# Optimization experiments

Hardware: AMD Instinct MI355X
Metric: run time of the kernel (lower is better)

## Reference

```python
import jax, jax.numpy as jnp
import numpy as np

BN_INV = 1.0 / np.sqrt(1.0 + 1e-5)  # eval-mode BatchNorm1d with running_mean=0, running_var=1


def _lin_bn_relu(x, W, g, b):
    # Linear(no bias) -> BN(eval) -> ReLU
    return jax.nn.relu((x @ W.T) * (g * BN_INV) + b)


def setup_inputs() -> dict:
    key = jax.random.key(0)
    ks = jax.random.split(key, 24)
    B, P, N, C, H, OUT = 8, 1024, 20, 32, 256, 256
    s = 0.05
    inp = {
        "polylines": jax.random.normal(ks[0], (B, P, N, C), dtype=jnp.float32),
        "polylines_mask": jax.random.randint(ks[1], (B, P, N), 0, 2) > 0,
        # pre_mlps: [Lin(C->H,no bias)+BN+ReLU] x2, Lin(H->H, bias)
        "pre_w0": jax.random.normal(ks[2], (H, C), dtype=jnp.float32) * s,
        "pre_g0": jnp.ones((H,), jnp.float32),
        "pre_b0": jnp.zeros((H,), jnp.float32),
        "pre_w1": jax.random.normal(ks[3], (H, H), dtype=jnp.float32) * s,
        "pre_g1": jnp.ones((H,), jnp.float32),
        "pre_b1": jnp.zeros((H,), jnp.float32),
        "pre_w2": jax.random.normal(ks[4], (H, H), dtype=jnp.float32) * s,
        "pre_bias2": jnp.zeros((H,), jnp.float32),
        # mlps: c_in=2H -> [H,H,H]
        "mlp_w0": jax.random.normal(ks[5], (H, 2 * H), dtype=jnp.float32) * s,
        "mlp_g0": jnp.ones((H,), jnp.float32),
        "mlp_b0": jnp.zeros((H,), jnp.float32),
        "mlp_w1": jax.random.normal(ks[6], (H, H), dtype=jnp.float32) * s,
        "mlp_g1": jnp.ones((H,), jnp.float32),
        "mlp_b1": jnp.zeros((H,), jnp.float32),
        "mlp_w2": jax.random.normal(ks[7], (H, H), dtype=jnp.float32) * s,
        "mlp_bias2": jnp.zeros((H,), jnp.float32),
        # out_mlps (without_norm): Lin(H->H,bias)+ReLU, Lin(H->OUT,bias)
        "out_w0": jax.random.normal(ks[8], (H, H), dtype=jnp.float32) * s,
        "out_b0": jnp.zeros((H,), jnp.float32),
        "out_w1": jax.random.normal(ks[9], (OUT, H), dtype=jnp.float32) * s,
        "out_b1": jnp.zeros((OUT,), jnp.float32),
    }
    return inp


def reference(polylines, polylines_mask,
              pre_w0, pre_g0, pre_b0, pre_w1, pre_g1, pre_b1, pre_w2, pre_bias2,
              mlp_w0, mlp_g0, mlp_b0, mlp_w1, mlp_g1, mlp_b1, mlp_w2, mlp_bias2,
              out_w0, out_b0, out_w1, out_b1):
    # gather->MLP->zero-scatter is equivalent to dense MLP followed by mask-zeroing
    # (all per-point ops are elementwise / last-dim matmuls).
    m = polylines_mask[..., None].astype(polylines.dtype)  # (B,P,N,1)

    x = _lin_bn_relu(polylines, pre_w0, pre_g0, pre_b0)
    x = _lin_bn_relu(x, pre_w1, pre_g1, pre_b1)
    x = (x @ pre_w2.T + pre_bias2) * m                      # (B,P,N,H) zero at invalid

    pooled = x.max(axis=2)                                  # (B,P,H) max over zero-filled buffer
    x = jnp.concatenate(
        [x, jnp.broadcast_to(pooled[:, :, None, :], x.shape)], axis=-1)  # (B,P,N,2H)

    x = _lin_bn_relu(x, mlp_w0, mlp_g0, mlp_b0)
    x = _lin_bn_relu(x, mlp_w1, mlp_g1, mlp_b1)
    x = (x @ mlp_w2.T + mlp_bias2) * m                      # (B,P,N,H)

    buf = x.max(axis=2)                                     # (B,P,H)

    valid = jnp.any(polylines_mask, axis=-1)                # sum(mask)>0
    y = jax.nn.relu(buf @ out_w0.T + out_b0)
    y = (y @ out_w1.T + out_b1) * valid[..., None].astype(buf.dtype)  # (B,P,OUT)
    return y
```

## Files before the change

### kernel.cpp

```cpp
#include <hip/hip_runtime.h>
#include <stdint.h>
#include <stddef.h>

typedef __bf16 bf16;
typedef __bf16 bf16x4 __attribute__((ext_vector_type(4)));
typedef __bf16 bf16x8 __attribute__((ext_vector_type(8)));
typedef float f32x4 __attribute__((ext_vector_type(4)));
typedef float f32x16 __attribute__((ext_vector_type(16)));

#define BNI 0.9999950000374996f
#define NROW 240
#define NPOLYB 12
#define TOTROW 163840
#define NPOLY 8192
#define NBLK 683

#define AADDR(r, ch) ((r)*256 + ((((ch) ^ ((r)&31)))<<3))

#define OFF_ACT  0
#define OFF_WB0  122880
#define OFF_T2   155648
#define OFF_VAL  161792
#define LDS_TOTAL 161840

#define WS_PRE_W0 0
#define WS_PRE_W1 8192
#define WS_PRE_W2 73728
#define WS_MLP_W0 139264
#define WS_MLP_W1 270336
#define WS_MLP_W2 335872
#define WS_OUT_W0 401408
#define WS_OUT_W1 466944

__device__ __forceinline__ bf16 f2b(float f){
  unsigned int i = __builtin_bit_cast(unsigned int, f);
  unsigned int r = i + 0x7fffu + ((i >> 16) & 1u);
  unsigned short h = (unsigned short)(r >> 16);
  return __builtin_bit_cast(bf16, h);
}
__device__ __forceinline__ float b2f(bf16 x){
  unsigned short u = __builtin_bit_cast(unsigned short, x);
  union { unsigned int i; float f; } v; v.i = ((unsigned int)u) << 16; return v.f;
}
__device__ __forceinline__ bf16x8 ld8f(const float* p, float sc){
  f32x4 a = *(const f32x4*)p;
  f32x4 b = *(const f32x4*)(p + 4);
  bf16x8 r;
  #pragma unroll
  for (int j = 0; j < 4; ++j){ r[j] = f2b(a[j]*sc); r[4+j] = f2b(b[j]*sc); }
  return r;
}

__global__ __launch_bounds__(256)
void prep_kernel(const float* s0, const float* s1, const float* s2, const float* s3,
                 const float* s4, const float* s5, const float* s6, const float* s7,
                 const float* g0, const float* g1, const float* g3, const float* g4,
                 bf16* dst)
{
  const int offs[8] = {WS_PRE_W0, WS_PRE_W1, WS_PRE_W2, WS_MLP_W0,
                       WS_MLP_W1, WS_MLP_W2, WS_OUT_W0, WS_OUT_W1};
  const int sz[8]   = {8192, 65536, 65536, 131072, 65536, 65536, 65536, 65536};
  const int ld[8]   = {32, 256, 256, 512, 256, 256, 256, 256};
  int r = blockIdx.y;
  const float* src = s0;
  if (r == 1) src = s1; else if (r == 2) src = s2; else if (r == 3) src = s3;
  else if (r == 4) src = s4; else if (r == 5) src = s5; else if (r == 6) src = s6;
  else if (r == 7) src = s7;
  const float* gp = (r==0)?g0:(r==1)?g1:(r==3)?g3:(r==4)?g4:nullptr;
  int i = (blockIdx.x*256 + threadIdx.x)*8;
  if (i < sz[r]){
    float sc = gp ? gp[i/ld[r]]*BNI : 1.0f;
    *(bf16x8*)&dst[offs[r] + i] = ld8f(src + i, sc);
  }
}

__device__ __forceinline__ void stageAsyncG2(const bf16* W, int ldK, int tile, int kh,
                                             bf16* buf, int rp, int lane){
  #pragma unroll
  for (int i = 0; i < 2; ++i){
    int id = rp*128 + i*64 + lane;
    int fr = id >> 4, kcd = id & 15;
    int kcs = kcd ^ (fr & 15);
    const bf16* gsrc = W + (size_t)(tile*32 + fr)*ldK + kh*128 + kcs*8;
    bf16* l = buf + (size_t)(rp*128 + i*64)*8;
    __builtin_amdgcn_global_load_lds(
        (const __attribute__((address_space(1))) void*)gsrc,
        (__attribute__((address_space(3))) void*)l,
        16, 0, 0);
  }
}

template<int RELU, int MASK, int ADDT2>
__device__ __forceinline__ void epiT(
    const f32x16& acc, int nt, int row, int poly, float mk, bool valid,
    bf16* sAct, const bf16* sT2, const float* bptr, int hi)
{
  #pragma unroll
  for (int q2 = 0; q2 < 4; ++q2){
    int f0 = nt*32 + 8*q2 + 4*hi;
    f32x4 bb = *(const f32x4*)(bptr + f0);
    bf16x4 tv = {};
    if (ADDT2) tv = *(const bf16x4*)&sT2[poly*256 + f0];
    bf16x4 o;
    #pragma unroll
    for (int j = 0; j < 4; ++j){
      float v = acc[4*q2 + j];
      if (ADDT2) v += b2f(tv[j]);
      v += bb[j];
      if (RELU) v = fmaxf(v, 0.0f);
      if (MASK) v *= mk;
      o[j] = f2b(v);
    }
    if (valid)
      *(bf16x4*)&sAct[row*256 + (((nt*4 + q2) ^ (row & 31))<<3) + 4*hi] = o;
  }
}

template<int RELU, int MASK, int ADDT2>
__device__ __forceinline__ void layerR2(
    bf16* sAct, bf16* wbase, const bf16* sT2,
    const bf16* W, int ldK, const float* bptr,
    const int* maskp, int blk, int g, int rp, int row0, int row1,
    int rowc0, int rowc1, int lane32, int hi, int lane)
{
  bf16x8 B0[16], B1[16];
  #pragma unroll
  for (int t = 0; t < 16; ++t){
    B0[t] = *(const bf16x8*)&sAct[AADDR(rowc0, 2*t + hi)];
    B1[t] = *(const bf16x8*)&sAct[AADDR(rowc1, 2*t + hi)];
  }
  float mk0 = 1.0f, mk1 = 1.0f;
  if (MASK){
    int g0 = blk*NROW + row0, g1 = blk*NROW + row1;
    mk0 = (row0 < NROW && g0 < TOTROW && maskp[g0]) ? 1.0f : 0.0f;
    mk1 = (row1 < NROW && g1 < TOTROW && maskp[g1]) ? 1.0f : 0.0f;
  }
  const int poly0 = rowc0/20, poly1 = rowc1/20;
  const bool valid0 = row0 < NROW, valid1 = row1 < NROW;
  bf16* bufA = wbase + (size_t)(2*g)*4096;
  bf16* bufB = bufA + 4096;

  stageAsyncG2(W, ldK, g*4, 0, bufA, rp, lane);
  __syncthreads();
  #pragma unroll 1
  for (int p = 0; p < 4; ++p){
    f32x16 acc0, acc1;
    stageAsyncG2(W, ldK, g*4 + p, 1, bufB, rp, lane);
    {
      const bf16* base = bufA + lane32*128;
      #pragma unroll
      for (int j = 0; j < 16; ++j){ acc0[j] = 0.0f; acc1[j] = 0.0f; }
      #pragma unroll
      for (int t = 0; t < 8; ++t){
        bf16x8 wf = *(const bf16x8*)(base + (((2*t + hi) ^ (lane32 & 15))<<3));
        acc0 = __builtin_amdgcn_mfma_f32_32x32x16_bf16(wf, B0[t], acc0, 0, 0, 0);
        acc1 = __builtin_amdgcn_mfma_f32_32x32x16_bf16(wf, B1[t], acc1, 0, 0, 0);
      }
    }
    __syncthreads();
    if (p < 3) stageAsyncG2(W, ldK, g*4 + p + 1, 0, bufA, rp, lane);
    {
      const bf16* base = bufB + lane32*128;
      #pragma unroll
      for (int t = 0; t < 8; ++t){
        bf16x8 wf = *(const bf16x8*)(base + (((2*t + hi) ^ (lane32 & 15))<<3));
        acc0 = __builtin_amdgcn_mfma_f32_32x32x16_bf16(wf, B0[8 + t], acc0, 0, 0, 0);
        acc1 = __builtin_amdgcn_mfma_f32_32x32x16_bf16(wf, B1[8 + t], acc1, 0, 0, 0);
      }
      epiT<RELU,MASK,ADDT2>(acc0, g*4 + p, row0, poly0, mk0, valid0, sAct, sT2, bptr, hi);
      epiT<RELU,MASK,ADDT2>(acc1, g*4 + p, row1, poly1, mk1, valid1, sAct, sT2, bptr, hi);
    }
    __syncthreads();
  }
}

__device__ __forceinline__ void poolT(const bf16* sAct, bf16* sPool, int tid){
  if (tid < 384){
    int poly = tid >> 5, c = tid & 31;
    float m[8];
    bf16x8 v0 = *(const bf16x8*)&sAct[AADDR(poly*20, c)];
    #pragma unroll
    for (int j = 0; j < 8; ++j) m[j] = b2f(v0[j]);
    for (int r = 1; r < 20; ++r){
      bf16x8 v = *(const bf16x8*)&sAct[AADDR(poly*20 + r, c)];
      #pragma unroll
      for (int j = 0; j < 8; ++j) m[j] = fmaxf(m[j], b2f(v[j]));
    }
    bf16x8 o;
    #pragma unroll
    for (int j = 0; j < 8; ++j) o[j] = f2b(m[j]);
    *(bf16x8*)&sPool[AADDR(poly, c)] = o;
  }
}

__global__ __launch_bounds__(512) __attribute__((amdgpu_waves_per_eu(1, 2)))
void traj_kernel(const float* __restrict__ poly, const int* __restrict__ maskp,
                 const float* pre_b0, const float* pre_b1, const float* pre_bias2,
                 const float* mlp_b0, const float* mlp_b1, const float* mlp_bias2,
                 const float* out_b0, const float* out_b1,
                 const bf16* __restrict__ ws,
                 float* __restrict__ outp)
{
  extern __shared__ char smem[];
  bf16*  sAct   = (bf16*)(smem + OFF_ACT);
  bf16*  wbase  = (bf16*)(smem + OFF_WB0);
  bf16*  sT2    = (bf16*)(smem + OFF_T2);
  float* sValid = (float*)(smem + OFF_VAL);
  bf16*  sPool  = wbase;
  bf16*  sY     = sAct;

  const int tid = threadIdx.x;
  const int w = tid >> 6, L = tid & 63, lane32 = L & 31, hi = L >> 5;
  const int g = w >> 2, rp = w & 3;
  const int row0 = rp*64 + lane32;
  const int row1 = row0 + 32;
  const int rowc0 = row0 < NROW ? row0 : NROW - 1;
  const int rowc1 = row1 < NROW ? row1 : NROW - 1;
  const int blk = blockIdx.x;

  const bf16* pw0 = ws + WS_PRE_W0;
  const bf16* pw1 = ws + WS_PRE_W1;
  const bf16* pw2 = ws + WS_PRE_W2;
  const bf16* mw0 = ws + WS_MLP_W0;
  const bf16* mw1 = ws + WS_MLP_W1;
  const bf16* mw2 = ws + WS_MLP_W2;
  const bf16* ow0 = ws + WS_OUT_W0;
  const bf16* ow1 = ws + WS_OUT_W1;

  #pragma unroll
  for (int i = 0; i < 2; ++i){
    int id = tid + 512*i;
    if (id < 960){
      int r = id >> 2, c = id & 3;
      int grow = blk*NROW + r;
      bf16x8 v = {};
      if (grow < TOTROW) v = ld8f(poly + (size_t)grow*32 + c*8, 1.0f);
      *(bf16x8*)&sAct[AADDR(r, c)] = v;
    }
  }
  __syncthreads();
  if (tid < NPOLYB){
    float v = 0.0f;
    #pragma unroll
    for (int r = 0; r < 20; ++r){
      int gg = blk*NROW + tid*20 + r;
      if (gg < TOTROW && maskp[gg]) v = 1.0f;
    }
    sValid[tid] = v;
  }

  {
    bf16x8 B00 = *(const bf16x8*)&sAct[AADDR(rowc0, hi)];
    bf16x8 B01 = *(const bf16x8*)&sAct[AADDR(rowc0, 2 + hi)];
    bf16x8 B10 = *(const bf16x8*)&sAct[AADDR(rowc1, hi)];
    bf16x8 B11 = *(const bf16x8*)&sAct[AADDR(rowc1, 2 + hi)];
    __syncthreads();
    #pragma unroll 1
    for (int ntl = 0; ntl < 4; ++ntl){
      int nt = g*4 + ntl;
      const bf16* p = pw0 + (size_t)(nt*32 + lane32)*32 + 8*hi;
      bf16x8 w0 = *(const bf16x8*)p;
      bf16x8 w1 = *(const bf16x8*)(p + 16);
      f32x16 acc0 = {}, acc1 = {};
      acc0 = __builtin_amdgcn_mfma_f32_32x32x16_bf16(w0, B00, acc0, 0, 0, 0);
      acc0 = __builtin_amdgcn_mfma_f32_32x32x16_bf16(w1, B01, acc0, 0, 0, 0);
      acc1 = __builtin_amdgcn_mfma_f32_32x32x16_bf16(w0, B10, acc1, 0, 0, 0);
      acc1 = __builtin_amdgcn_mfma_f32_32x32x16_bf16(w1, B11, acc1, 0, 0, 0);
      epiT<1,0,0>(acc0, nt, row0, 0, 1.0f, row0 < NROW, sAct, sT2, pre_b0, hi);
      epiT<1,0,0>(acc1, nt, row1, 0, 1.0f, row1 < NROW, sAct, sT2, pre_b0, hi);
    }
  }
  __syncthreads();

  layerR2<1,0,0>(sAct, wbase, sT2, pw1, 256, pre_b1,    maskp, blk, g, rp, row0, row1, rowc0, rowc1, lane32, hi, L);
  layerR2<0,1,0>(sAct, wbase, sT2, pw2, 256, pre_bias2, maskp, blk, g, rp, row0, row1, rowc0, rowc1, lane32, hi, L);

  poolT(sAct, sPool, tid);
  __syncthreads();

  {
    bf16x8 Bp[16];
    #pragma unroll
    for (int t = 0; t < 16; ++t)
      Bp[t] = *(const bf16x8*)&sPool[AADDR((lane32 < NPOLYB ? lane32 : 0), 2*t + hi)];
    int nt = w;
    const bf16* p = mw0 + (size_t)(nt*32 + lane32)*512 + 256 + 8*hi;
    f32x16 acc = {};
    #pragma unroll
    for (int t = 0; t < 16; ++t){
      bf16x8 wf = *(const bf16x8*)(p + 16*t);
      acc = __builtin_amdgcn_mfma_f32_32x32x16_bf16(wf, Bp[t], acc, 0, 0, 0);
    }
    if (lane32 < NPOLYB){
      #pragma unroll
      for (int q2 = 0; q2 < 4; ++q2){
        int f0 = nt*32 + 8*q2 + 4*hi;
        bf16x4 o;
        #pragma unroll
        for (int j = 0; j < 4; ++j) o[j] = f2b(acc[4*q2 + j]);
        *(bf16x4*)&sT2[lane32*256 + f0] = o;
      }
    }
  }
  __syncthreads();

  layerR2<1,0,1>(sAct, wbase, sT2, mw0, 512, mlp_b0,    maskp, blk, g, rp, row0, row1, rowc0, rowc1, lane32, hi, L);
  layerR2<1,0,0>(sAct, wbase, sT2, mw1, 256, mlp_b1,    maskp, blk, g, rp, row0, row1, rowc0, rowc1, lane32, hi, L);
  layerR2<0,1,0>(sAct, wbase, sT2, mw2, 256, mlp_bias2, maskp, blk, g, rp, row0, row1, rowc0, rowc1, lane32, hi, L);

  poolT(sAct, sPool, tid);
  __syncthreads();

  {
    bf16x8 Bp[16];
    #pragma unroll
    for (int t = 0; t < 16; ++t)
      Bp[t] = *(const bf16x8*)&sPool[AADDR((lane32 < NPOLYB ? lane32 : 0), 2*t + hi)];
    int nt = w;
    const bf16* p = ow0 + (size_t)(nt*32 + lane32)*256 + 8*hi;
    f32x16 acc = {};
    #pragma unroll
    for (int t = 0; t < 16; ++t){
      bf16x8 wf = *(const bf16x8*)(p + 16*t);
      acc = __builtin_amdgcn_mfma_f32_32x32x16_bf16(wf, Bp[t], acc, 0, 0, 0);
    }
    if (lane32 < NPOLYB){
      #pragma unroll
      for (int q2 = 0; q2 < 4; ++q2){
        int f0 = nt*32 + 8*q2 + 4*hi;
        f32x4 bb = *(const f32x4*)(out_b0 + f0);
        bf16x4 o;
        #pragma unroll
        for (int j = 0; j < 4; ++j) o[j] = f2b(fmaxf(acc[4*q2 + j] + bb[j], 0.0f));
        *(bf16x4*)&sY[lane32*256 + (((nt*4 + q2) ^ (lane32 & 31))<<3) + 4*hi] = o;
      }
    }
  }
  __syncthreads();

  {
    bf16x8 By[16];
    #pragma unroll
    for (int t = 0; t < 16; ++t)
      By[t] = *(const bf16x8*)&sY[AADDR((lane32 < NPOLYB ? lane32 : 0), 2*t + hi)];
    int gp = blk*NPOLYB + lane32;
    float vd = (lane32 < NPOLYB) ? sValid[lane32] : 0.0f;
    int nt = w;
    const bf16* p = ow1 + (size_t)(nt*32 + lane32)*256 + 8*hi;
    f32x16 acc = {};
    #pragma unroll
    for (int t = 0; t < 16; ++t){
      bf16x8 wf = *(const bf16x8*)(p + 16*t);
      acc = __builtin_amdgcn_mfma_f32_32x32x16_bf16(wf, By[t], acc, 0, 0, 0);
    }
    if (lane32 < NPOLYB && gp < NPOLY){
      #pragma unroll
      for (int q2 = 0; q2 < 4; ++q2){
        int f0 = nt*32 + 8*q2 + 4*hi;
        f32x4 bb = *(const f32x4*)(out_b1 + f0);
        f32x4 o;
        #pragma unroll
        for (int j = 0; j < 4; ++j) o[j] = (acc[4*q2 + j] + bb[j]) * vd;
        *(f32x4*)&outp[(size_t)gp*256 + f0] = o;
      }
    }
  }
}

extern "C" void kernel_launch(void* const* d_in, const int* in_sizes, int n_in,
                              void* d_out, int out_size, void* d_ws, size_t ws_size,
                              hipStream_t stream)
{
  const float* poly      = (const float*)d_in[0];
  const int*   maskp     = (const int*)  d_in[1];
  const float* pre_w0    = (const float*)d_in[2];
  const float* pre_g0    = (const float*)d_in[3];
  const float* pre_b0    = (const float*)d_in[4];
  const float* pre_w1    = (const float*)d_in[5];
  const float* pre_g1    = (const float*)d_in[6];
  const float* pre_b1    = (const float*)d_in[7];
  const float* pre_w2    = (const float*)d_in[8];
  const float* pre_bias2 = (const float*)d_in[9];
  const float* mlp_w0    = (const float*)d_in[10];
  const float* mlp_g0    = (const float*)d_in[11];
  const float* mlp_b0    = (const float*)d_in[12];
  const float* mlp_w1    = (const float*)d_in[13];
  const float* mlp_g1    = (const float*)d_in[14];
  const float* mlp_b1    = (const float*)d_in[15];
  const float* mlp_w2    = (const float*)d_in[16];
  const float* mlp_bias2 = (const float*)d_in[17];
  const float* out_w0    = (const float*)d_in[18];
  const float* out_b0    = (const float*)d_in[19];
  const float* out_w1    = (const float*)d_in[20];
  const float* out_b1    = (const float*)d_in[21];

  bf16* ws = (bf16*)d_ws;

  (void)hipFuncSetAttribute((const void*)&traj_kernel,
                            hipFuncAttributeMaxDynamicSharedMemorySize, LDS_TOTAL);

  prep_kernel<<<dim3(64, 8), dim3(256), 0, stream>>>(
      pre_w0, pre_w1, pre_w2, mlp_w0, mlp_w1, mlp_w2, out_w0, out_w1,
      pre_g0, pre_g1, mlp_g0, mlp_g1, ws);

  traj_kernel<<<dim3(NBLK), dim3(512), LDS_TOTAL, stream>>>(
      poly, maskp,
      pre_b0, pre_b1, pre_bias2,
      mlp_b0, mlp_b1, mlp_bias2,
      out_b0, out_b1,
      ws, (float*)d_out);
}
```

Before: 325.8 us.

## Halve block tile to 120 rows with 256 threads and quarter-K weight staging

Each block now processes 6 polylines (120 rows) with 4 waves instead of 12 polylines with 8 waves. LDS use drops to about 80KB, so two blocks can fit per CU, and the grid doubles to 1366 blocks. Weight tiles are now staged in four 64-wide K chunks with smaller double buffers. Each wave also loops over two output column tiles in the pooled and output stages. The intent is higher occupancy and better latency hiding, at the cost of more barriers per layer and weights being reloaded across twice as many blocks.

```diff
diff --git a/kernel.cpp b/kernel.cpp
--- a/kernel.cpp
+++ b/kernel.cpp
@@ -9,19 +9,19 @@
 typedef float f32x16 __attribute__((ext_vector_type(16)));
 
 #define BNI 0.9999950000374996f
-#define NROW 240
-#define NPOLYB 12
+#define NROW 120
+#define NPOLYB 6
 #define TOTROW 163840
 #define NPOLY 8192
-#define NBLK 683
+#define NBLK 1366
 
 #define AADDR(r, ch) ((r)*256 + ((((ch) ^ ((r)&31)))<<3))
 
 #define OFF_ACT  0
-#define OFF_WB0  122880
-#define OFF_T2   155648
-#define OFF_VAL  161792
-#define LDS_TOTAL 161840
+#define OFF_WB   61440
+#define OFF_T2   77824
+#define OFF_VAL  80896
+#define LDS_TOTAL 80920
 
 #define WS_PRE_W0 0
 #define WS_PRE_W1 8192
@@ -74,19 +74,32 @@
   }
 }
 
-__device__ __forceinline__ void stageAsyncG2(const bf16* W, int ldK, int tile, int kh,
-                                             bf16* buf, int rp, int lane){
+__device__ __forceinline__ void stageAsyncQ(const bf16* W, int ldK, int tile, int kq,
+                                            bf16* buf, int rp, int lane){
   #pragma unroll
   for (int i = 0; i < 2; ++i){
     int id = rp*128 + i*64 + lane;
-    int fr = id >> 4, kcd = id & 15;
-    int kcs = kcd ^ (fr & 15);
-    const bf16* gsrc = W + (size_t)(tile*32 + fr)*ldK + kh*128 + kcs*8;
+    int fr = id >> 3, kcd = id & 7;
+    int kcs = kcd ^ (fr & 7);
+    const bf16* gsrc = W + (size_t)(tile*32 + fr)*ldK + kq*64 + kcs*8;
     bf16* l = buf + (size_t)(rp*128 + i*64)*8;
     __builtin_amdgcn_global_load_lds(
         (const __attribute__((address_space(1))) void*)gsrc,
         (__attribute__((address_space(3))) void*)l,
         16, 0, 0);
+  }
+}
+
+template<int KQ>
+__device__ __forceinline__ void mfma4(const bf16* buf, int lane32, int hi,
+                                      const bf16x8 (&B0)[16], const bf16x8 (&B1)[16],
+                                      f32x16& acc0, f32x16& acc1){
+  const bf16* base = buf + lane32*64;
+  #pragma unroll
+  for (int s = 0; s < 4; ++s){
+    bf16x8 wf = *(const bf16x8*)(base + (((2*s + hi) ^ (lane32 & 7))<<3));
+    acc0 = __builtin_amdgcn_mfma_f32_32x32x16_bf16(wf, B0[4*KQ + s], acc0, 0, 0, 0);
+    acc1 = __builtin_amdgcn_mfma_f32_32x32x16_bf16(wf, B1[4*KQ + s], acc1, 0, 0, 0);
   }
 }
 
@@ -117,7 +130,7 @@
 }
 
 template<int RELU, int MASK, int ADDT2>
-__device__ __forceinline__ void layerR2(
+__device__ __forceinline__ void layerQ(
     bf16* sAct, bf16* wbase, const bf16* sT2,
     const bf16* W, int ldK, const float* bptr,
     const int* maskp, int blk, int g, int rp, int row0, int row1,
@@ -137,45 +150,35 @@
   }
   const int poly0 = rowc0/20, poly1 = rowc1/20;
   const bool valid0 = row0 < NROW, valid1 = row1 < NROW;
-  bf16* bufA = wbase + (size_t)(2*g)*4096;
-  bf16* bufB = bufA + 4096;
-
-  stageAsyncG2(W, ldK, g*4, 0, bufA, rp, lane);
+  bf16* bufA = wbase + (size_t)(2*g)*2048;
+  bf16* bufB = bufA + 2048;
+
+  stageAsyncQ(W, ldK, g*4, 0, bufA, rp, lane);
   __syncthreads();
   #pragma unroll 1
   for (int p = 0; p < 4; ++p){
     f32x16 acc0, acc1;
-    stageAsyncG2(W, ldK, g*4 + p, 1, bufB, rp, lane);
-    {
-      const bf16* base = bufA + lane32*128;
-      #pragma unroll
-      for (int j = 0; j < 16; ++j){ acc0[j] = 0.0f; acc1[j] = 0.0f; }
-      #pragma unroll
-      for (int t = 0; t < 8; ++t){
-        bf16x8 wf = *(const bf16x8*)(base + (((2*t + hi) ^ (lane32 & 15))<<3));
-        acc0 = __builtin_amdgcn_mfma_f32_32x32x16_bf16(wf, B0[t], acc0, 0, 0, 0);
-        acc1 = __builtin_amdgcn_mfma_f32_32x32x16_bf16(wf, B1[t], acc1, 0, 0, 0);
-      }
-    }
+    #pragma unroll
+    for (int j = 0; j < 16; ++j){ acc0[j] = 0.0f; acc1[j] = 0.0f; }
+    stageAsyncQ(W, ldK, g*4 + p, 1, bufB, rp, lane);
+    mfma4<0>(bufA, lane32, hi, B0, B1, acc0, acc1);
     __syncthreads();
-    if (p < 3) stageAsyncG2(W, ldK, g*4 + p + 1, 0, bufA, rp, lane);
-    {
-      const bf16* base = bufB + lane32*128;
-      #pragma unroll
-      for (int t = 0; t < 8; ++t){
-        bf16x8 wf = *(const bf16x8*)(base + (((2*t + hi) ^ (lane32 & 15))<<3));
-        acc0 = __builtin_amdgcn_mfma_f32_32x32x16_bf16(wf, B0[8 + t], acc0, 0, 0, 0);
-        acc1 = __builtin_amdgcn_mfma_f32_32x32x16_bf16(wf, B1[8 + t], acc1, 0, 0, 0);
-      }
-      epiT<RELU,MASK,ADDT2>(acc0, g*4 + p, row0, poly0, mk0, valid0, sAct, sT2, bptr, hi);
-      epiT<RELU,MASK,ADDT2>(acc1, g*4 + p, row1, poly1, mk1, valid1, sAct, sT2, bptr, hi);
-    }
+    stageAsyncQ(W, ldK, g*4 + p, 2, bufA, rp, lane);
+    mfma4<1>(bufB, lane32, hi, B0, B1, acc0, acc1);
     __syncthreads();
+    stageAsyncQ(W, ldK, g*4 + p, 3, bufB, rp, lane);
+    mfma4<2>(bufA, lane32, hi, B0, B1, acc0, acc1);
+    __syncthreads();
+    if (p < 3) stageAsyncQ(W, ldK, g*4 + p + 1, 0, bufA, rp, lane);
+    mfma4<3>(bufB, lane32, hi, B0, B1, acc0, acc1);
+    epiT<RELU,MASK,ADDT2>(acc0, g*4 + p, row0, poly0, mk0, valid0, sAct, sT2, bptr, hi);
+    epiT<RELU,MASK,ADDT2>(acc1, g*4 + p, row1, poly1, mk1, valid1, sAct, sT2, bptr, hi);
+    __syncthreads();
   }
 }
 
 __device__ __forceinline__ void poolT(const bf16* sAct, bf16* sPool, int tid){
-  if (tid < 384){
+  if (tid < 192){
     int poly = tid >> 5, c = tid & 31;
     float m[8];
     bf16x8 v0 = *(const bf16x8*)&sAct[AADDR(poly*20, c)];
@@ -193,7 +196,7 @@
   }
 }
 
-__global__ __launch_bounds__(512) __attribute__((amdgpu_waves_per_eu(1, 2)))
+__global__ __launch_bounds__(256) __attribute__((amdgpu_waves_per_eu(1, 2)))
 void traj_kernel(const float* __restrict__ poly, const int* __restrict__ maskp,
                  const float* pre_b0, const float* pre_b1, const float* pre_bias2,
                  const float* mlp_b0, const float* mlp_b1, const float* mlp_bias2,
@@ -203,7 +206,7 @@
 {
   extern __shared__ char smem[];
   bf16*  sAct   = (bf16*)(smem + OFF_ACT);
-  bf16*  wbase  = (bf16*)(smem + OFF_WB0);
+  bf16*  wbase  = (bf16*)(smem + OFF_WB);
   bf16*  sT2    = (bf16*)(smem + OFF_T2);
   float* sValid = (float*)(smem + OFF_VAL);
   bf16*  sPool  = wbase;
@@ -211,7 +214,7 @@
 
   const int tid = threadIdx.x;
   const int w = tid >> 6, L = tid & 63, lane32 = L & 31, hi = L >> 5;
-  const int g = w >> 2, rp = w & 3;
+  const int g = w >> 1, rp = w & 1;
   const int row0 = rp*64 + lane32;
   const int row1 = row0 + 32;
   const int rowc0 = row0 < NROW ? row0 : NROW - 1;
@@ -229,8 +232,8 @@
 
   #pragma unroll
   for (int i = 0; i < 2; ++i){
-    int id = tid + 512*i;
-    if (id < 960){
+    int id = tid + 256*i;
+    if (id < 480){
       int r = id >> 2, c = id & 3;
       int grow = blk*NROW + r;
       bf16x8 v = {};
@@ -272,8 +275,8 @@
   }
   __syncthreads();
 
-  layerR2<1,0,0>(sAct, wbase, sT2, pw1, 256, pre_b1,    maskp, blk, g, rp, row0, row1, rowc0, rowc1, lane32, hi, L);
-  layerR2<0,1,0>(sAct, wbase, sT2, pw2, 256, pre_bias2, maskp, blk, g, rp, row0, row1, rowc0, rowc1, lane32, hi, L);
+  layerQ<1,0,0>(sAct, wbase, sT2, pw1, 256, pre_b1,    maskp, blk, g, rp, row0, row1, rowc0, rowc1, lane32, hi, L);
+  layerQ<0,1,0>(sAct, wbase, sT2, pw2, 256, pre_bias2, maskp, blk, g, rp, row0, row1, rowc0, rowc1, lane32, hi, L);
 
   poolT(sAct, sPool, tid);
   __syncthreads();
@@ -283,30 +286,33 @@
     #pragma unroll
     for (int t = 0; t < 16; ++t)
       Bp[t] = *(const bf16x8*)&sPool[AADDR((lane32 < NPOLYB ? lane32 : 0), 2*t + hi)];
-    int nt = w;
-    const bf16* p = mw0 + (size_t)(nt*32 + lane32)*512 + 256 + 8*hi;
-    f32x16 acc = {};
-    #pragma unroll
-    for (int t = 0; t < 16; ++t){
-      bf16x8 wf = *(const bf16x8*)(p + 16*t);
-      acc = __builtin_amdgcn_mfma_f32_32x32x16_bf16(wf, Bp[t], acc, 0, 0, 0);
-    }
-    if (lane32 < NPOLYB){
+    #pragma unroll 1
+    for (int it = 0; it < 2; ++it){
+      int nt = w + 4*it;
+      const bf16* p = mw0 + (size_t)(nt*32 + lane32)*512 + 256 + 8*hi;
+      f32x16 acc = {};
       #pragma unroll
-      for (int q2 = 0; q2 < 4; ++q2){
-        int f0 = nt*32 + 8*q2 + 4*hi;
-        bf16x4 o;
+      for (int t = 0; t < 16; ++t){
+        bf16x8 wf = *(const bf16x8*)(p + 16*t);
+        acc = __builtin_amdgcn_mfma_f32_32x32x16_bf16(wf, Bp[t], acc, 0, 0, 0);
+      }
+      if (lane32 < NPOLYB){
         #pragma unroll
-        for (int j = 0; j < 4; ++j) o[j] = f2b(acc[4*q2 + j]);
-        *(bf16x4*)&sT2[lane32*256 + f0] = o;
-      }
-    }
-  }
-  __syncthreads();
-
-  layerR2<1,0,1>(sAct, wbase, sT2, mw0, 512, mlp_b0,    maskp, blk, g, rp, row0, row1, rowc0, rowc1, lane32, hi, L);
-  layerR2<1,0,0>(sAct, wbase, sT2, mw1, 256, mlp_b1,    maskp, blk, g, rp, row0, row1, rowc0, rowc1, lane32, hi, L);
-  layerR2<0,1,0>(sAct, wbase, sT2, mw2, 256, mlp_bias2, maskp, blk, g, rp, row0, row1, rowc0, rowc1, lane32, hi, L);
+        for (int q2 = 0; q2 < 4; ++q2){
+          int f0 = nt*32 + 8*q2 + 4*hi;
+          bf16x4 o;
+          #pragma unroll
+          for (int j = 0; j < 4; ++j) o[j] = f2b(acc[4*q2 + j]);
+          *(bf16x4*)&sT2[lane32*256 + f0] = o;
+        }
+      }
+    }
+  }
+  __syncthreads();
+
+  layerQ<1,0,1>(sAct, wbase, sT2, mw0, 512, mlp_b0,    maskp, blk, g, rp, row0, row1, rowc0, rowc1, lane32, hi, L);
+  layerQ<1,0,0>(sAct, wbase, sT2, mw1, 256, mlp_b1,    maskp, blk, g, rp, row0, row1, rowc0, rowc1, lane32, hi, L);
+  layerQ<0,1,0>(sAct, wbase, sT2, mw2, 256, mlp_bias2, maskp, blk, g, rp, row0, row1, rowc0, rowc1, lane32, hi, L);
 
   poolT(sAct, sPool, tid);
   __syncthreads();
@@ -316,23 +322,26 @@
     #pragma unroll
     for (int t = 0; t < 16; ++t)
       Bp[t] = *(const bf16x8*)&sPool[AADDR((lane32 < NPOLYB ? lane32 : 0), 2*t + hi)];
-    int nt = w;
-    const bf16* p = ow0 + (size_t)(nt*32 + lane32)*256 + 8*hi;
-    f32x16 acc = {};
-    #pragma unroll
-    for (int t = 0; t < 16; ++t){
-      bf16x8 wf = *(const bf16x8*)(p + 16*t);
-      acc = __builtin_amdgcn_mfma_f32_32x32x16_bf16(wf, Bp[t], acc, 0, 0, 0);
-    }
-    if (lane32 < NPOLYB){
+    #pragma unroll 1
+    for (int it = 0; it < 2; ++it){
+      int nt = w + 4*it;
+      const bf16* p = ow0 + (size_t)(nt*32 + lane32)*256 + 8*hi;
+      f32x16 acc = {};
       #pragma unroll
-      for (int q2 = 0; q2 < 4; ++q2){
-        int f0 = nt*32 + 8*q2 + 4*hi;
-        f32x4 bb = *(const f32x4*)(out_b0 + f0);
-        bf16x4 o;
+      for (int t = 0; t < 16; ++t){
+        bf16x8 wf = *(const bf16x8*)(p + 16*t);
+        acc = __builtin_amdgcn_mfma_f32_32x32x16_bf16(wf, Bp[t], acc, 0, 0, 0);
+      }
+      if (lane32 < NPOLYB){
         #pragma unroll
-        for (int j = 0; j < 4; ++j) o[j] = f2b(fmaxf(acc[4*q2 + j] + bb[j], 0.0f));
-        *(bf16x4*)&sY[lane32*256 + (((nt*4 + q2) ^ (lane32 & 31))<<3) + 4*hi] = o;
+        for (int q2 = 0; q2 < 4; ++q2){
+          int f0 = nt*32 + 8*q2 + 4*hi;
+          f32x4 bb = *(const f32x4*)(out_b0 + f0);
+          bf16x4 o;
+          #pragma unroll
+          for (int j = 0; j < 4; ++j) o[j] = f2b(fmaxf(acc[4*q2 + j] + bb[j], 0.0f));
+          *(bf16x4*)&sY[lane32*256 + (((nt*4 + q2) ^ (lane32 & 31))<<3) + 4*hi] = o;
+        }
       }
     }
   }
@@ -345,23 +354,26 @@
       By[t] = *(const bf16x8*)&sY[AADDR((lane32 < NPOLYB ? lane32 : 0), 2*t + hi)];
     int gp = blk*NPOLYB + lane32;
     float vd = (lane32 < NPOLYB) ? sValid[lane32] : 0.0f;
-    int nt = w;
-    const bf16* p = ow1 + (size_t)(nt*32 + lane32)*256 + 8*hi;
-    f32x16 acc = {};
-    #pragma unroll
-    for (int t = 0; t < 16; ++t){
-      bf16x8 wf = *(const bf16x8*)(p + 16*t);
-      acc = __builtin_amdgcn_mfma_f32_32x32x16_bf16(wf, By[t], acc, 0, 0, 0);
-    }
-    if (lane32 < NPOLYB && gp < NPOLY){
+    #pragma unroll 1
+    for (int it = 0; it < 2; ++it){
+      int nt = w + 4*it;
+      const bf16* p = ow1 + (size_t)(nt*32 + lane32)*256 + 8*hi;
+      f32x16 acc = {};
       #pragma unroll
-      for (int q2 = 0; q2 < 4; ++q2){
-        int f0 = nt*32 + 8*q2 + 4*hi;
-        f32x4 bb = *(const f32x4*)(out_b1 + f0);
-        f32x4 o;
+      for (int t = 0; t < 16; ++t){
+        bf16x8 wf = *(const bf16x8*)(p + 16*t);
+        acc = __builtin_amdgcn_mfma_f32_32x32x16_bf16(wf, By[t], acc, 0, 0, 0);
+      }
+      if (lane32 < NPOLYB && gp < NPOLY){
         #pragma unroll
-        for (int j = 0; j < 4; ++j) o[j] = (acc[4*q2 + j] + bb[j]) * vd;
-        *(f32x4*)&outp[(size_t)gp*256 + f0] = o;
+        for (int q2 = 0; q2 < 4; ++q2){
+          int f0 = nt*32 + 8*q2 + 4*hi;
+          f32x4 bb = *(const f32x4*)(out_b1 + f0);
+          f32x4 o;
+          #pragma unroll
+          for (int j = 0; j < 4; ++j) o[j] = (acc[4*q2 + j] + bb[j]) * vd;
+          *(f32x4*)&outp[(size_t)gp*256 + f0] = o;
+        }
       }
     }
   }
@@ -403,7 +415,7 @@
       pre_w0, pre_w1, pre_w2, mlp_w0, mlp_w1, mlp_w2, out_w0, out_w1,
       pre_g0, pre_g1, mlp_g0, mlp_g1, ws);
 
-  traj_kernel<<<dim3(NBLK), dim3(512), LDS_TOTAL, stream>>>(
+  traj_kernel<<<dim3(NBLK), dim3(256), LDS_TOTAL, stream>>>(
       poly, maskp,
       pre_b0, pre_b1, pre_bias2,
       mlp_b0, mlp_b1, mlp_bias2,
```

Result: slower. 448.8 us (+37.8%).
